# Optimization experiments

Hardware: AMD Instinct MI355X
Metric: run time of the kernel (lower is better)

Reference implementation:

```python
import jax, jax.numpy as jnp
import numpy as np

B, NH, T, H, W = 2, 4, 8, 14, 14
DIM = 384
HD = DIM // NH  # 96 = head_dim = depthwise conv channels
N = T * H * W  # 1568 tokens, no cls
EPS = 1e-6


def _dwconv3d(x, w):
    # x: [BN, C, T, H, W], w: [C, 1, 3, 3, 3]; depthwise conv, stride 1, pad 1
    return jax.lax.conv_general_dilated(
        x, w, window_strides=(1, 1, 1), padding=[(1, 1)] * 3,
        feature_group_count=x.shape[1],
        dimension_numbers=('NCDHW', 'OIDHW', 'NCDHW'))


def _layernorm(x, g, b):
    m = jnp.mean(x, axis=-1, keepdims=True)
    v = jnp.var(x, axis=-1, keepdims=True)
    return (x - m) * jax.lax.rsqrt(v + EPS) * g + b


def _attention_pool(x4, conv_w, ln_g, ln_b, t, h, w):
    # x4: [B, nh, L, c] with L = t*h*w (no cls token)
    Bq, n, L, c = x4.shape
    y = x4.reshape(Bq * n, t, h, w, c).transpose(0, 4, 1, 2, 3)  # [(b nh), c, t, h, w]
    y = _dwconv3d(y, conv_w)
    y = y.transpose(0, 2, 3, 4, 1).reshape(Bq, n, L, c)
    return _layernorm(y, ln_g, ln_b)


def setup_inputs() -> dict:
    key = jax.random.key(0)
    ks = jax.random.split(key, 12)
    inp = {
        'x': jax.random.normal(ks[0], (B, N, DIM), jnp.float32),
        'qkv_w': jax.random.normal(ks[1], (3 * DIM, DIM), jnp.float32) * 0.02,
        'proj_w': jax.random.normal(ks[2], (DIM, DIM), jnp.float32) * 0.02,
        'proj_b': jnp.zeros((DIM,), jnp.float32),
        'pool_q_w': jax.random.normal(ks[3], (HD, 1, 3, 3, 3), jnp.float32) * 0.1,
        'pool_k_w': jax.random.normal(ks[4], (HD, 1, 3, 3, 3), jnp.float32) * 0.1,
        'pool_v_w': jax.random.normal(ks[5], (HD, 1, 3, 3, 3), jnp.float32) * 0.1,
        'norm_q_w': jnp.ones((HD,), jnp.float32), 'norm_q_b': jnp.zeros((HD,), jnp.float32),
        'norm_k_w': jnp.ones((HD,), jnp.float32), 'norm_k_b': jnp.zeros((HD,), jnp.float32),
        'norm_v_w': jnp.ones((HD,), jnp.float32), 'norm_v_b': jnp.zeros((HD,), jnp.float32),
        'rel_pos_h': jax.random.normal(ks[6], (2 * H - 1, HD), jnp.float32) * 0.02,
        'rel_pos_w': jax.random.normal(ks[7], (2 * W - 1, HD), jnp.float32) * 0.02,
        'rel_pos_t': jax.random.normal(ks[8], (2 * T - 1, HD), jnp.float32) * 0.02,
        't': T, 'h': H, 'w': W,
    }
    return inp


def reference(x, qkv_w, proj_w, proj_b, pool_q_w, pool_k_w, pool_v_w,
              norm_q_w, norm_q_b, norm_k_w, norm_k_b, norm_v_w, norm_v_b,
              rel_pos_h, rel_pos_w, rel_pos_t, t, h, w):
    Bq, Nq, _ = x.shape
    # fused QKV projection (qkv_bias=False)
    qkv = (x @ qkv_w.T).reshape(Bq, Nq, 3, NH, HD).transpose(2, 0, 3, 1, 4)
    q, k, v = qkv[0], qkv[1], qkv[2]  # [B, nh, N, hd]
    # pooled Q/K/V: depthwise conv3d + LayerNorm (stride 1 -> shapes preserved)
    q = _attention_pool(q, pool_q_w, norm_q_w, norm_q_b, t, h, w)
    k = _attention_pool(k, pool_k_w, norm_k_w, norm_k_b, t, h, w)
    v = _attention_pool(v, pool_v_w, norm_v_w, norm_v_b, t, h, w)

    scale = HD ** -0.5
    attn = jnp.einsum('bnqc,bnkc->bnqk', q * scale, k)  # [B, nh, N, N]

    # decomposed relative position biases (q_shape == k_shape, ratios == 1)
    dist_h = jnp.arange(h)[:, None] - jnp.arange(h)[None, :] + (h - 1)
    dist_w = jnp.arange(w)[:, None] - jnp.arange(w)[None, :] + (w - 1)
    dist_t = jnp.arange(t)[:, None] - jnp.arange(t)[None, :] + (t - 1)
    Rh = rel_pos_h[dist_h]  # [h, h, c]
    Rw = rel_pos_w[dist_w]  # [w, w, c]
    Rt = rel_pos_t[dist_t]  # [t, t, c]

    r_q = q.reshape(Bq, NH, t, h, w, HD)
    rel_h = jnp.einsum('bnthwc,hkc->bnthwk', r_q, Rh)  # [B,nh,t,h,w,kh]
    rel_w = jnp.einsum('bnthwc,wkc->bnthwk', r_q, Rw)  # [B,nh,t,h,w,kw]
    rel_t = jnp.einsum('bnthwc,tkc->bnthwk', r_q, Rt)  # [B,nh,t,h,w,kt]

    attn8 = attn.reshape(Bq, NH, t, h, w, t, h, w)
    attn8 = (attn8
             + rel_h[:, :, :, :, :, None, :, None]
             + rel_w[:, :, :, :, :, None, None, :]
             + rel_t[:, :, :, :, :, :, None, None])
    attn = jax.nn.softmax(attn8.reshape(Bq, NH, Nq, Nq), axis=-1)

    out = jnp.einsum('bnqk,bnkc->bnqc', attn, v)
    out = out + q  # residual pooling
    out = out.transpose(0, 2, 1, 3).reshape(Bq, Nq, DIM)
    out = out @ proj_w.T + proj_b
    return out
```

## Files before the change

kernel.cpp:

```cpp
#include <hip/hip_runtime.h>

#define B_    2
#define NH_   4
#define T_    8
#define H_    14
#define W_    14
#define HW_   196
#define HD_   96
#define DIM_  384
#define N_    1568
#define BH_   (B_*NH_)
#define BN_   (B_*N_)
#define BHN_  (BH_*N_)
#define CAUG_ 160

typedef unsigned short bf_t;
typedef unsigned int   u32;
typedef __attribute__((ext_vector_type(8))) short bf16x8;
typedef __attribute__((ext_vector_type(4))) float f32x4;

#define LOG2E 1.4426950408889634f
#define QSCALE_LOG2E 0.14724445f

static __device__ __forceinline__ float lo16(u32 v){ union{u32 i; float f;}x; x.i = v<<16;           return x.f; }
static __device__ __forceinline__ float hi16(u32 v){ union{u32 i; float f;}x; x.i = v & 0xffff0000u; return x.f; }
static __device__ __forceinline__ float b2f(bf_t v){ union{u32 i; float f;}x; x.i = ((u32)v)<<16;    return x.f; }
static __device__ __forceinline__ bf_t  f2b(float f){
  union{float f; u32 i;} x; x.f = f;
  return (bf_t)((x.i + 0x7fffu + ((x.i>>16)&1u)) >> 16);
}
static __device__ __forceinline__ u32 pack2(float a, float b){
  return (u32)f2b(a) | ((u32)f2b(b) << 16);
}

#define NA_ (BN_*DIM_)
#define NB_ (3*DIM_*DIM_)
#define NC_ (DIM_*DIM_)
#define CAST_BLOCKS ((NA_+NB_+NC_)/4/256)

__global__ __launch_bounds__(256) void k_cast(
    const float* __restrict__ a, bf_t* __restrict__ ad,
    const float* __restrict__ b, bf_t* __restrict__ bd,
    const float* __restrict__ c, bf_t* __restrict__ cd,
    const float* __restrict__ wq, const float* __restrict__ wk,
    const float* __restrict__ wv, float* __restrict__ tq,
    float* __restrict__ tk, float* __restrict__ tv){
  if (blockIdx.x < CAST_BLOCKS){
    const int i = blockIdx.x*256 + threadIdx.x;
    const int i4 = i*4;
    const float4* src; bf_t* dst; int off;
    if (i4 < NA_)           { src = (const float4*)a; dst = ad; off = i; }
    else if (i4 < NA_+NB_)  { src = (const float4*)b; dst = bd; off = i - NA_/4; }
    else                    { src = (const float4*)c; dst = cd; off = i - (NA_+NB_)/4; }
    const float4 v = src[off];
    ushort4 o; o.x = f2b(v.x); o.y = f2b(v.y); o.z = f2b(v.z); o.w = f2b(v.w);
    ((ushort4*)dst)[off] = o;
  } else {
    const int idx = (blockIdx.x - CAST_BLOCKS)*256 + threadIdx.x;
    if (idx >= 3*HD_*27) return;
    const int t = idx / (HD_*27), rem = idx % (HD_*27);
    const int ch = rem / 27, j = rem % 27;
    const float* s = (t==0)? wq : (t==1)? wk : wv;
    float* d       = (t==0)? tq : (t==1)? tk : tv;
    d[j*HD_ + ch] = s[ch*27 + j];
  }
}

__global__ __launch_bounds__(256) void k_qkv(const bf_t* __restrict__ Xb,
    const bf_t* __restrict__ Wb,
    bf_t* __restrict__ q, bf_t* __restrict__ k, bf_t* __restrict__ v){
  const int wid = threadIdx.x >> 6, lane = threadIdx.x & 63;
  const int wr = wid & 1, wc = wid >> 1;
  const int nl = lane & 15, quad = lane >> 4;
  const int r0 = blockIdx.x*64 + wr*32;
  const int c0 = blockIdx.y*128 + wc*64;
  f32x4 acc[2][4];
  #pragma unroll
  for (int i = 0; i < 2; ++i)
    #pragma unroll
    for (int j = 0; j < 4; ++j) acc[i][j] = (f32x4){0.f,0.f,0.f,0.f};
  const bf_t* A0 = Xb + (size_t)(r0 + nl)*DIM_ + quad*8;
  const bf_t* B0 = Wb + (size_t)(c0 + nl)*DIM_ + quad*8;
  #pragma unroll 2
  for (int k0 = 0; k0 < 12; ++k0){
    const bf16x8 a0 = *(const bf16x8*)(A0 + k0*32);
    const bf16x8 a1 = *(const bf16x8*)(A0 + 16*DIM_ + k0*32);
    bf16x8 bf[4];
    #pragma unroll
    for (int j = 0; j < 4; ++j) bf[j] = *(const bf16x8*)(B0 + (size_t)j*16*DIM_ + k0*32);
    #pragma unroll
    for (int j = 0; j < 4; ++j){
      acc[0][j] = __builtin_amdgcn_mfma_f32_16x16x32_bf16(a0, bf[j], acc[0][j], 0, 0, 0);
      acc[1][j] = __builtin_amdgcn_mfma_f32_16x16x32_bf16(a1, bf[j], acc[1][j], 0, 0, 0);
    }
  }
  #pragma unroll
  for (int i = 0; i < 2; ++i){
    #pragma unroll
    for (int r = 0; r < 4; ++r){
      const int m  = r0 + i*16 + quad*4 + r;
      const int bb = m / N_, nn = m % N_;
      #pragma unroll
      for (int j = 0; j < 4; ++j){
        const int col = c0 + j*16 + nl;
        const int s = col / DIM_, rem = col - s*DIM_;
        const int head = rem / HD_, hc = rem % HD_;
        bf_t* dst = (s==0) ? q : (s==1) ? k : v;
        dst[((size_t)(bb*NH_ + head)*N_ + nn)*HD_ + hc] = f2b(acc[i][j][r]);
      }
    }
  }
}

static __device__ __forceinline__ void ln_butterfly(
    float v0, float v1, float& mean, float& rstd){
  float s  = v0 + v1;
  float s2 = v0*v0 + v1*v1;
  #pragma unroll
  for (int off = 32; off > 0; off >>= 1){
    s  += __shfl_xor(s,  off);
    s2 += __shfl_xor(s2, off);
  }
  mean = s * (1.f/HD_);
  const float var = fmaxf(s2*(1.f/HD_) - mean*mean, 0.f);
  rstd = rsqrtf(var + 1e-6f);
}

__global__ __launch_bounds__(256) void k_pool_slab(
    const bf_t* __restrict__ qr_, const bf_t* __restrict__ kr_, const bf_t* __restrict__ vr_,
    const float* __restrict__ wtq, const float* __restrict__ wtk, const float* __restrict__ wtv,
    const float* __restrict__ gq, const float* __restrict__ bq,
    const float* __restrict__ gk, const float* __restrict__ bk,
    const float* __restrict__ gv, const float* __restrict__ bv,
    const float* __restrict__ rph, const float* __restrict__ rpw,
    const float* __restrict__ rpt,
    bf_t* __restrict__ qp, bf_t* __restrict__ Qaug,
    bf_t* __restrict__ Kt, bf_t* __restrict__ Vtt){
  __shared__ __align__(16) bf_t slab[90][HD_];
  __shared__ float qtmp[4][2][HD_];
  __shared__ u32 vres[8][48];
  const int wid = threadIdx.x >> 6, lane = threadIdx.x & 63;
  const int sec = blockIdx.x / 1568;
  const int rr_ = blockIdx.x % 1568;
  const int bh = rr_ / 196, tok0 = (rr_ % 196)*8;
  const bf_t*  src = (sec==0)? qr_ : (sec==1)? kr_ : vr_;
  const float* wt  = (sec==0)? wtq : (sec==1)? wtk : wtv;
  const float* g   = (sec==0)? gq  : (sec==1)? gk  : gv;
  const float* be  = (sec==0)? bq  : (sec==1)? bk  : bv;
  const bf_t* base = src + (size_t)bh*N_*HD_;

  for (int li = threadIdx.x; li < 90*12; li += 256){
    const int rw = li / 12, ss = li % 12;
    const int dt = rw/30 - 1, dh = (rw%30)/10 - 1, dwp = rw%10 - 1;
    int nn = tok0 + dt*HW_ + dh*W_ + dwp;
    nn = min(max(nn, 0), N_-1);
    *(uint4*)&slab[rw][ss*8] = *(const uint4*)(base + (size_t)nn*HD_ + ss*8);
  }
  __syncthreads();

  const int c0 = (lane < 48) ? 2*lane : 0;
  float2 wgt[27];
  #pragma unroll
  for (int j = 0; j < 27; ++j) wgt[j] = *(const float2*)(wt + j*HD_ + c0);
  const float gg0 = g[c0], gg1 = g[c0+1], be0 = be[c0], be1 = be[c0+1];

  #pragma unroll
  for (int tk = 0; tk < 2; ++tk){
    const int u = wid*2 + tk;
    const int n = tok0 + u;
    const int tt = n / HW_; const int rm = n % HW_;
    const int hh = rm / W_, ww = rm % W_;
    float v0 = 0.f, v1 = 0.f;
    #pragma unroll
    for (int j = 0; j < 27; ++j){
      const int dt = j/9 - 1, dh = (j%9)/3 - 1, dw = j%3 - 1;
      const bool ok = ((unsigned)(tt+dt) < (unsigned)T_)
                   && ((unsigned)(hh+dh) < (unsigned)H_)
                   && ((unsigned)(ww+dw) < (unsigned)W_);
      const int rj = (dt+1)*30 + (dh+1)*10 + (dw + u + 1);
      u32 d = *(const u32*)&slab[rj][c0];
      d = ok ? d : 0u;
      v0 = fmaf(wgt[j].x, lo16(d), v0);
      v1 = fmaf(wgt[j].y, hi16(d), v1);
    }
    if (lane >= 48){ v0 = 0.f; v1 = 0.f; }
    float mean, rstd;
    ln_butterfly(v0, v1, mean, rstd);
    const float y0 = (v0 - mean)*rstd*gg0 + be0;
    const float y1 = (v1 - mean)*rstd*gg1 + be1;

    if (sec == 0){
      const int token = bh*N_ + n;
      if (lane < 48){
        ((u32*)qp)  [(size_t)token*48 + lane] = pack2(y0, y1);
        ((u32*)Qaug)[(size_t)token*80 + lane] = pack2(y0*QSCALE_LOG2E, y1*QSCALE_LOG2E);
        qtmp[wid][tk][c0] = y0; qtmp[wid][tk][c0+1] = y1;
      }
      __syncthreads();
      if (lane < 36){
        const float* tb; int idx;
        if (lane < 14)      { tb = rph; idx = hh - lane      + 13; }
        else if (lane < 28) { tb = rpw; idx = ww - (lane-14) + 13; }
        else                { tb = rpt; idx = tt - (lane-28) +  7; }
        const float4* t4 = (const float4*)(tb + (size_t)idx*HD_);
        float acc = 0.f;
        #pragma unroll
        for (int i = 0; i < 24; ++i){
          const float4 rv = t4[i];
          acc += qtmp[wid][tk][4*i]*rv.x + qtmp[wid][tk][4*i+1]*rv.y
               + qtmp[wid][tk][4*i+2]*rv.z + qtmp[wid][tk][4*i+3]*rv.w;
        }
        Qaug[(size_t)token*CAUG_ + HD_ + lane] = f2b(acc * LOG2E);
      } else if (lane < 64){
        Qaug[(size_t)token*CAUG_ + HD_ + lane] = 0;
      }
    } else if (sec == 1){
      const int tl = n >> 4, nr = n & 15;
      if (lane < 48){
        const size_t idx = ((((size_t)bh*98 + tl)*5 + (lane>>4))*64
                           + ((lane&15)>>2)*16 + nr)*4 + (lane&3);
        ((u32*)Kt)[idx] = pack2(y0, y1);
      } else {
        const int m = lane - 48;
        u32 pr_[2];
        #pragma unroll
        for (int h2 = 0; h2 < 2; ++h2){
          u32 w_ = 0;
          #pragma unroll
          for (int e = 0; e < 2; ++e){
            const int jj = 4*m + 2*h2 + e;
            bool on = (jj < 14) ? (jj == hh) : (jj < 28) ? (jj-14 == ww)
                     : (jj < 36) ? (jj-28 == tt) : false;
            if (on) w_ |= (0x3F80u << (16*e));
          }
          pr_[h2] = w_;
        }
        const size_t bidx = ((((size_t)bh*98 + tl)*5 + (3 + (m>>3)))*64
                            + ((m&7)>>1)*16 + nr)*4 + 2*(m&1);
        *(uint2*)((u32*)Kt + bidx) = make_uint2(pr_[0], pr_[1]);
      }
    } else {
      if (lane < 48) vres[u][lane] = pack2(y0, y1);
    }
  }

  if (sec == 2){
    __syncthreads();
    if (threadIdx.x < HD_){
      const int c = threadIdx.x;
      u32 o[4];
      #pragma unroll
      for (int i = 0; i < 4; ++i){
        const u32 a = vres[2*i][c>>1], b = vres[2*i+1][c>>1];
        const u32 ra = (c&1) ? (a >> 16) : (a & 0xffffu);
        const u32 rb = (c&1) ? (b >> 16) : (b & 0xffffu);
        o[i] = ra | (rb << 16);
      }
      const int pr = tok0 >> 5, qd = (tok0 & 31) >> 3;
      bf_t* dst = Vtt + ((((size_t)bh*49 + pr)*6 + (c>>4))*64 + qd*16 + (c&15))*8;
      *(uint4*)dst = make_uint4(o[0], o[1], o[2], o[3]);
    }
  }
}

__global__ __launch_bounds__(512) void k_attn(
    const bf_t* __restrict__ Qaug, const bf_t* __restrict__ Kt,
    const bf_t* __restrict__ Vtt, const bf_t* __restrict__ qp,
    bf_t* __restrict__ attb){
  __shared__ __align__(16) short Pb[8][16][40];
  __shared__ float Os[8][16][96];
  __shared__ float ms[8][16], ls[8][16];
  const int wid = threadIdx.x >> 6, lane = threadIdx.x & 63;
  const int bh = blockIdx.x / 98, qt = blockIdx.x % 98;
  const int q0 = qt*16;
  const int nl = lane & 15, quad = lane >> 4;

  bf16x8 qa[5];
  {
    const bf_t* Qrow = Qaug + ((size_t)bh*N_ + q0 + nl)*CAUG_ + quad*8;
    #pragma unroll
    for (int i = 0; i < 5; ++i) qa[i] = *(const bf16x8*)(Qrow + i*32);
  }
  short* Pw = &Pb[wid][0][0];

  f32x4 O[6];
  #pragma unroll
  for (int i = 0; i < 6; ++i) O[i] = (f32x4){0.f,0.f,0.f,0.f};
  float mc[4]   = {0.f,0.f,0.f,0.f};
  float rmax[4] = {-3e38f,-3e38f,-3e38f,-3e38f};
  float l[4]    = {0.f,0.f,0.f,0.f};

  auto s_tile = [&](int tl, int half){
    const bf_t* Kp = Kt + (((size_t)bh*98 + tl)*5*64 + lane)*8;
    f32x4 s = (f32x4){0.f,0.f,0.f,0.f};
    #pragma unroll
    for (int i = 0; i < 5; ++i)
      s = __builtin_amdgcn_mfma_f32_16x16x32_bf16(qa[i], *(const bf16x8*)(Kp + i*512), s, 0, 0, 0);
    #pragma unroll
    for (int r = 0; r < 4; ++r){
      rmax[r] = fmaxf(rmax[r], s[r]);
      const float p = exp2f(s[r] - mc[r]);
      l[r] += p;
      Pw[(quad*4 + r)*40 + half*16 + nl] = (short)f2b(p);
    }
  };
  auto rescale = [&](){
    #pragma unroll
    for (int r = 0; r < 4; ++r){
      float tm = rmax[r];
      tm = fmaxf(tm, __shfl_xor(tm, 1));
      tm = fmaxf(tm, __shfl_xor(tm, 2));
      tm = fmaxf(tm, __shfl_xor(tm, 4));
      tm = fmaxf(tm, __shfl_xor(tm, 8));
      const float mn = fmaxf(mc[r], tm);
      const float al = exp2f(mc[r] - mn);
      mc[r] = mn; l[r] *= al;
      #pragma unroll
      for (int ct = 0; ct < 6; ++ct) O[ct][r] *= al;
    }
  };

  const int p0 = (wid == 0) ? 0 : (7 + 6*(wid-1));
  const int npairs = (wid == 0) ? 7 : 6;
  #pragma unroll 1
  for (int pi = 0; pi < npairs; ++pi){
    const int kp = p0 + pi;
    s_tile(2*kp,     0);
    s_tile(2*kp + 1, 1);
    const bf16x8 pa = *(const bf16x8*)(Pw + nl*40 + quad*8);
    const bf_t* Vp = Vtt + (((size_t)bh*49 + kp)*6*64 + lane)*8;
    #pragma unroll
    for (int ct = 0; ct < 6; ++ct)
      O[ct] = __builtin_amdgcn_mfma_f32_16x16x32_bf16(pa, *(const bf16x8*)(Vp + ct*512), O[ct], 0, 0, 0);
    if (pi == npairs-1) rescale();
  }

  #pragma unroll
  for (int r = 0; r < 4; ++r){
    float ls_ = l[r];
    ls_ += __shfl_xor(ls_, 1); ls_ += __shfl_xor(ls_, 2);
    ls_ += __shfl_xor(ls_, 4); ls_ += __shfl_xor(ls_, 8);
    if (nl == 0){ ms[wid][quad*4 + r] = mc[r]; ls[wid][quad*4 + r] = ls_; }
    #pragma unroll
    for (int ct = 0; ct < 6; ++ct) Os[wid][quad*4 + r][ct*16 + nl] = O[ct][r];
  }
  __syncthreads();

  const int bb = bh >> 2, head = bh & 3;
  for (int e = threadIdx.x; e < 16*96; e += 512){
    const int row = e / 96, col = e % 96;
    float mx = -3e38f;
    #pragma unroll
    for (int w = 0; w < 8; ++w) mx = fmaxf(mx, ms[w][row]);
    float L = 0.f, A = 0.f;
    #pragma unroll
    for (int w = 0; w < 8; ++w){
      const float wt = exp2f(ms[w][row] - mx);
      L += wt*ls[w][row];
      A += wt*Os[w][row][col];
    }
    const int qg = q0 + row;
    const float val = A/L + b2f(qp[((size_t)bh*N_ + qg)*HD_ + col]);
    attb[((size_t)(bb*N_ + qg))*DIM_ + head*HD_ + col] = f2b(val);
  }
}

__global__ __launch_bounds__(256) void k_proj(const bf_t* __restrict__ Ab,
    const bf_t* __restrict__ Wpb, const float* __restrict__ pb,
    float* __restrict__ out){
  const int wid = threadIdx.x >> 6, lane = threadIdx.x & 63;
  const int wr = wid & 1, wc = wid >> 1;
  const int nl = lane & 15, quad = lane >> 4;
  const int r0 = blockIdx.x*64 + wr*32;
  const int c0 = blockIdx.y*128 + wc*64;
  f32x4 acc[2][4];
  #pragma unroll
  for (int i = 0; i < 2; ++i)
    #pragma unroll
    for (int j = 0; j < 4; ++j) acc[i][j] = (f32x4){0.f,0.f,0.f,0.f};
  const bf_t* A0 = Ab  + (size_t)(r0 + nl)*DIM_ + quad*8;
  const bf_t* B0 = Wpb + (size_t)(c0 + nl)*DIM_ + quad*8;
  #pragma unroll 2
  for (int k0 = 0; k0 < 12; ++k0){
    const bf16x8 a0 = *(const bf16x8*)(A0 + k0*32);
    const bf16x8 a1 = *(const bf16x8*)(A0 + 16*DIM_ + k0*32);
    bf16x8 bf[4];
    #pragma unroll
    for (int j = 0; j < 4; ++j) bf[j] = *(const bf16x8*)(B0 + (size_t)j*16*DIM_ + k0*32);
    #pragma unroll
    for (int j = 0; j < 4; ++j){
      acc[0][j] = __builtin_amdgcn_mfma_f32_16x16x32_bf16(a0, bf[j], acc[0][j], 0, 0, 0);
      acc[1][j] = __builtin_amdgcn_mfma_f32_16x16x32_bf16(a1, bf[j], acc[1][j], 0, 0, 0);
    }
  }
  #pragma unroll
  for (int i = 0; i < 2; ++i){
    #pragma unroll
    for (int r = 0; r < 4; ++r){
      const int m = r0 + i*16 + quad*4 + r;
      #pragma unroll
      for (int j = 0; j < 4; ++j){
        const int col = c0 + j*16 + nl;
        out[(size_t)m*DIM_ + col] = acc[i][j][r] + pb[col];
      }
    }
  }
}

extern "C" void kernel_launch(void* const* d_in, const int* in_sizes, int n_in,
                              void* d_out, int out_size, void* d_ws, size_t ws_size,
                              hipStream_t stream){
  const float* x      = (const float*)d_in[0];
  const float* qkv_w  = (const float*)d_in[1];
  const float* proj_w = (const float*)d_in[2];
  const float* proj_b = (const float*)d_in[3];
  const float* pqw    = (const float*)d_in[4];
  const float* pkw    = (const float*)d_in[5];
  const float* pvw    = (const float*)d_in[6];
  const float* nqw    = (const float*)d_in[7];
  const float* nqb    = (const float*)d_in[8];
  const float* nkw    = (const float*)d_in[9];
  const float* nkb    = (const float*)d_in[10];
  const float* nvw    = (const float*)d_in[11];
  const float* nvb    = (const float*)d_in[12];
  const float* rph    = (const float*)d_in[13];
  const float* rpw    = (const float*)d_in[14];
  const float* rpt    = (const float*)d_in[15];

  char* p = (char*)d_ws;
  const size_t RAW = (size_t)BH_*N_*HD_*2;
  const size_t AUG = (size_t)BH_*N_*CAUG_*2;
  bf_t* xb     = (bf_t*)(p);
  bf_t* wqkvb  = (bf_t*)(p + RAW);
  bf_t* wprojb = (bf_t*)(p + RAW + 884736);
  char* p2 = p + RAW + 884736 + 294912;
  bf_t* raw_q  = (bf_t*)(p2);
  bf_t* raw_k  = (bf_t*)(p2 + RAW);
  bf_t* raw_v  = (bf_t*)(p2 + 2*RAW);
  bf_t* attb   = raw_q;
  bf_t* qp     = (bf_t*)(p2 + 3*RAW);
  bf_t* Qaug   = (bf_t*)(p2 + 4*RAW);
  bf_t* Kt     = (bf_t*)(p2 + 4*RAW + AUG);
  bf_t* Vtt    = (bf_t*)(p2 + 4*RAW + 2*AUG);
  float* wtq   = (float*)(p2 + 4*RAW + 2*AUG + RAW);
  float* wtk   = wtq + 27*HD_;
  float* wtv   = wtk + 27*HD_;

  k_cast     <<<CAST_BLOCKS + 31, 256, 0, stream>>>(x, xb, qkv_w, wqkvb, proj_w, wprojb,
                                                    pqw, pkw, pvw, wtq, wtk, wtv);
  k_qkv      <<<dim3(BN_/64, 9),  256, 0, stream>>>(xb, wqkvb, raw_q, raw_k, raw_v);
  k_pool_slab<<<3*1568,           256, 0, stream>>>(raw_q, raw_k, raw_v,
                                                    wtq, wtk, wtv,
                                                    nqw, nqb, nkw, nkb, nvw, nvb,
                                                    rph, rpw, rpt,
                                                    qp, Qaug, Kt, Vtt);
  k_attn     <<<BH_*98,           512, 0, stream>>>(Qaug, Kt, Vtt, qp, attb);
  k_proj     <<<dim3(BN_/64, 3),  256, 0, stream>>>(attb, wprojb, proj_b, (float*)d_out);
}
```

Before: 221.1 us.

## Store GEMM operands in MFMA fragment-tiled layout and pool 16 tokens per block

```diff
diff --git a/kernel.cpp b/kernel.cpp
--- a/kernel.cpp
+++ b/kernel.cpp
@@ -32,6 +32,9 @@
 static __device__ __forceinline__ u32 pack2(float a, float b){
   return (u32)f2b(a) | ((u32)f2b(b) << 16);
 }
+static __device__ __forceinline__ size_t ftidx(int row, int k){
+  return ((((size_t)(row>>4))*12 + (k>>5))*64 + ((k>>3)&3)*16 + (row&15))*8 + (k&7);
+}
 
 #define NA_ (BN_*DIM_)
 #define NB_ (3*DIM_*DIM_)
@@ -48,13 +51,21 @@
   if (blockIdx.x < CAST_BLOCKS){
     const int i = blockIdx.x*256 + threadIdx.x;
     const int i4 = i*4;
-    const float4* src; bf_t* dst; int off;
-    if (i4 < NA_)           { src = (const float4*)a; dst = ad; off = i; }
-    else if (i4 < NA_+NB_)  { src = (const float4*)b; dst = bd; off = i - NA_/4; }
-    else                    { src = (const float4*)c; dst = cd; off = i - (NA_+NB_)/4; }
-    const float4 v = src[off];
+    float4 v; bf_t* dst; int row, k;
+    if (i4 < NA_){
+      v = ((const float4*)a)[i];
+      dst = ad; row = i4/DIM_; k = i4%DIM_;
+    } else if (i4 < NA_+NB_){
+      const int f = i4 - NA_;
+      v = ((const float4*)b)[i - NA_/4];
+      dst = bd; row = f/DIM_; k = f%DIM_;
+    } else {
+      const int f = i4 - NA_ - NB_;
+      v = ((const float4*)c)[i - (NA_+NB_)/4];
+      dst = cd; row = f/DIM_; k = f%DIM_;
+    }
     ushort4 o; o.x = f2b(v.x); o.y = f2b(v.y); o.z = f2b(v.z); o.w = f2b(v.w);
-    ((ushort4*)dst)[off] = o;
+    *(ushort4*)(dst + ftidx(row, k)) = o;
   } else {
     const int idx = (blockIdx.x - CAST_BLOCKS)*256 + threadIdx.x;
     if (idx >= 3*HD_*27) return;
@@ -66,28 +77,29 @@
   }
 }
 
-__global__ __launch_bounds__(256) void k_qkv(const bf_t* __restrict__ Xb,
-    const bf_t* __restrict__ Wb,
+__global__ __launch_bounds__(256) void k_qkv(const bf_t* __restrict__ Xt,
+    const bf_t* __restrict__ Wt,
     bf_t* __restrict__ q, bf_t* __restrict__ k, bf_t* __restrict__ v){
   const int wid = threadIdx.x >> 6, lane = threadIdx.x & 63;
   const int wr = wid & 1, wc = wid >> 1;
   const int nl = lane & 15, quad = lane >> 4;
   const int r0 = blockIdx.x*64 + wr*32;
-  const int c0 = blockIdx.y*128 + wc*64;
+  const int mt0 = r0 >> 4;
+  const int nt0 = blockIdx.y*8 + wc*4;
   f32x4 acc[2][4];
   #pragma unroll
   for (int i = 0; i < 2; ++i)
     #pragma unroll
     for (int j = 0; j < 4; ++j) acc[i][j] = (f32x4){0.f,0.f,0.f,0.f};
-  const bf_t* A0 = Xb + (size_t)(r0 + nl)*DIM_ + quad*8;
-  const bf_t* B0 = Wb + (size_t)(c0 + nl)*DIM_ + quad*8;
+  const bf_t* A0 = Xt + ((size_t)mt0*12*64 + lane)*8;
+  const bf_t* B0 = Wt + ((size_t)nt0*12*64 + lane)*8;
   #pragma unroll 2
   for (int k0 = 0; k0 < 12; ++k0){
-    const bf16x8 a0 = *(const bf16x8*)(A0 + k0*32);
-    const bf16x8 a1 = *(const bf16x8*)(A0 + 16*DIM_ + k0*32);
+    const bf16x8 a0 = *(const bf16x8*)(A0 + k0*512);
+    const bf16x8 a1 = *(const bf16x8*)(A0 + 12*512 + k0*512);
     bf16x8 bf[4];
     #pragma unroll
-    for (int j = 0; j < 4; ++j) bf[j] = *(const bf16x8*)(B0 + (size_t)j*16*DIM_ + k0*32);
+    for (int j = 0; j < 4; ++j) bf[j] = *(const bf16x8*)(B0 + (size_t)(j*12 + k0)*512);
     #pragma unroll
     for (int j = 0; j < 4; ++j){
       acc[0][j] = __builtin_amdgcn_mfma_f32_16x16x32_bf16(a0, bf[j], acc[0][j], 0, 0, 0);
@@ -102,7 +114,7 @@
       const int bb = m / N_, nn = m % N_;
       #pragma unroll
       for (int j = 0; j < 4; ++j){
-        const int col = c0 + j*16 + nl;
+        const int col = (nt0 + j)*16 + nl;
         const int s = col / DIM_, rem = col - s*DIM_;
         const int head = rem / HD_, hc = rem % HD_;
         bf_t* dst = (s==0) ? q : (s==1) ? k : v;
@@ -136,23 +148,23 @@
     const float* __restrict__ rpt,
     bf_t* __restrict__ qp, bf_t* __restrict__ Qaug,
     bf_t* __restrict__ Kt, bf_t* __restrict__ Vtt){
-  __shared__ __align__(16) bf_t slab[90][HD_];
-  __shared__ float qtmp[4][2][HD_];
-  __shared__ u32 vres[8][48];
+  __shared__ __align__(16) bf_t slab[162][HD_];
+  __shared__ float qtmp[4][4][HD_];
+  __shared__ u32 vres[16][48];
   const int wid = threadIdx.x >> 6, lane = threadIdx.x & 63;
-  const int sec = blockIdx.x / 1568;
-  const int rr_ = blockIdx.x % 1568;
-  const int bh = rr_ / 196, tok0 = (rr_ % 196)*8;
+  const int sec = blockIdx.x / 784;
+  const int rr_ = blockIdx.x % 784;
+  const int bh = rr_ / 98, tok0 = (rr_ % 98)*16;
   const bf_t*  src = (sec==0)? qr_ : (sec==1)? kr_ : vr_;
   const float* wt  = (sec==0)? wtq : (sec==1)? wtk : wtv;
   const float* g   = (sec==0)? gq  : (sec==1)? gk  : gv;
   const float* be  = (sec==0)? bq  : (sec==1)? bk  : bv;
   const bf_t* base = src + (size_t)bh*N_*HD_;
 
-  for (int li = threadIdx.x; li < 90*12; li += 256){
+  for (int li = threadIdx.x; li < 162*12; li += 256){
     const int rw = li / 12, ss = li % 12;
-    const int dt = rw/30 - 1, dh = (rw%30)/10 - 1, dwp = rw%10 - 1;
-    int nn = tok0 + dt*HW_ + dh*W_ + dwp;
+    const int aa = rw/54, bb2 = (rw%54)/18, cc = rw%18;
+    int nn = tok0 + (aa-1)*HW_ + (bb2-1)*W_ + (cc-1);
     nn = min(max(nn, 0), N_-1);
     *(uint4*)&slab[rw][ss*8] = *(const uint4*)(base + (size_t)nn*HD_ + ss*8);
   }
@@ -164,9 +176,9 @@
   for (int j = 0; j < 27; ++j) wgt[j] = *(const float2*)(wt + j*HD_ + c0);
   const float gg0 = g[c0], gg1 = g[c0+1], be0 = be[c0], be1 = be[c0+1];
 
-  #pragma unroll
-  for (int tk = 0; tk < 2; ++tk){
-    const int u = wid*2 + tk;
+  #pragma unroll 1
+  for (int tk = 0; tk < 4; ++tk){
+    const int u = wid*4 + tk;
     const int n = tok0 + u;
     const int tt = n / HW_; const int rm = n % HW_;
     const int hh = rm / W_, ww = rm % W_;
@@ -177,7 +189,7 @@
       const bool ok = ((unsigned)(tt+dt) < (unsigned)T_)
                    && ((unsigned)(hh+dh) < (unsigned)H_)
                    && ((unsigned)(ww+dw) < (unsigned)W_);
-      const int rj = (dt+1)*30 + (dh+1)*10 + (dw + u + 1);
+      const int rj = (dt+1)*54 + (dh+1)*18 + (dw + u + 1);
       u32 d = *(const u32*)&slab[rj][c0];
       d = ok ? d : 0u;
       v0 = fmaf(wgt[j].x, lo16(d), v0);
@@ -246,17 +258,19 @@
 
   if (sec == 2){
     __syncthreads();
-    if (threadIdx.x < HD_){
-      const int c = threadIdx.x;
+    if (threadIdx.x < 2*HD_){
+      const int grp = threadIdx.x / HD_, c = threadIdx.x % HD_;
+      const int t0g = grp*8;
       u32 o[4];
       #pragma unroll
       for (int i = 0; i < 4; ++i){
-        const u32 a = vres[2*i][c>>1], b = vres[2*i+1][c>>1];
+        const u32 a = vres[t0g + 2*i][c>>1], b = vres[t0g + 2*i+1][c>>1];
         const u32 ra = (c&1) ? (a >> 16) : (a & 0xffffu);
         const u32 rb = (c&1) ? (b >> 16) : (b & 0xffffu);
         o[i] = ra | (rb << 16);
       }
-      const int pr = tok0 >> 5, qd = (tok0 & 31) >> 3;
+      const int n0g = tok0 + t0g;
+      const int pr = n0g >> 5, qd = (n0g & 31) >> 3;
       bf_t* dst = Vtt + ((((size_t)bh*49 + pr)*6 + (c>>4))*64 + qd*16 + (c&15))*8;
       *(uint4*)dst = make_uint4(o[0], o[1], o[2], o[3]);
     }
@@ -347,6 +361,7 @@
   __syncthreads();
 
   const int bb = bh >> 2, head = bh & 3;
+  const int grow0 = bb*N_ + q0;
   for (int e = threadIdx.x; e < 16*96; e += 512){
     const int row = e / 96, col = e % 96;
     float mx = -3e38f;
@@ -359,34 +374,34 @@
       L += wt*ls[w][row];
       A += wt*Os[w][row][col];
     }
-    const int qg = q0 + row;
-    const float val = A/L + b2f(qp[((size_t)bh*N_ + qg)*HD_ + col]);
-    attb[((size_t)(bb*N_ + qg))*DIM_ + head*HD_ + col] = f2b(val);
-  }
-}
-
-__global__ __launch_bounds__(256) void k_proj(const bf_t* __restrict__ Ab,
-    const bf_t* __restrict__ Wpb, const float* __restrict__ pb,
+    const float val = A/L + b2f(qp[((size_t)bh*N_ + q0 + row)*HD_ + col]);
+    attb[ftidx(grow0 + row, head*HD_ + col)] = f2b(val);
+  }
+}
+
+__global__ __launch_bounds__(256) void k_proj(const bf_t* __restrict__ At,
+    const bf_t* __restrict__ Wpt, const float* __restrict__ pb,
     float* __restrict__ out){
   const int wid = threadIdx.x >> 6, lane = threadIdx.x & 63;
   const int wr = wid & 1, wc = wid >> 1;
   const int nl = lane & 15, quad = lane >> 4;
   const int r0 = blockIdx.x*64 + wr*32;
-  const int c0 = blockIdx.y*128 + wc*64;
+  const int mt0 = r0 >> 4;
+  const int nt0 = blockIdx.y*8 + wc*4;
   f32x4 acc[2][4];
   #pragma unroll
   for (int i = 0; i < 2; ++i)
     #pragma unroll
     for (int j = 0; j < 4; ++j) acc[i][j] = (f32x4){0.f,0.f,0.f,0.f};
-  const bf_t* A0 = Ab  + (size_t)(r0 + nl)*DIM_ + quad*8;
-  const bf_t* B0 = Wpb + (size_t)(c0 + nl)*DIM_ + quad*8;
+  const bf_t* A0 = At  + ((size_t)mt0*12*64 + lane)*8;
+  const bf_t* B0 = Wpt + ((size_t)nt0*12*64 + lane)*8;
   #pragma unroll 2
   for (int k0 = 0; k0 < 12; ++k0){
-    const bf16x8 a0 = *(const bf16x8*)(A0 + k0*32);
-    const bf16x8 a1 = *(const bf16x8*)(A0 + 16*DIM_ + k0*32);
+    const bf16x8 a0 = *(const bf16x8*)(A0 + k0*512);
+    const bf16x8 a1 = *(const bf16x8*)(A0 + 12*512 + k0*512);
     bf16x8 bf[4];
     #pragma unroll
-    for (int j = 0; j < 4; ++j) bf[j] = *(const bf16x8*)(B0 + (size_t)j*16*DIM_ + k0*32);
+    for (int j = 0; j < 4; ++j) bf[j] = *(const bf16x8*)(B0 + (size_t)(j*12 + k0)*512);
     #pragma unroll
     for (int j = 0; j < 4; ++j){
       acc[0][j] = __builtin_amdgcn_mfma_f32_16x16x32_bf16(a0, bf[j], acc[0][j], 0, 0, 0);
@@ -400,7 +415,7 @@
       const int m = r0 + i*16 + quad*4 + r;
       #pragma unroll
       for (int j = 0; j < 4; ++j){
-        const int col = c0 + j*16 + nl;
+        const int col = (nt0 + j)*16 + nl;
         out[(size_t)m*DIM_ + col] = acc[i][j][r] + pb[col];
       }
     }
@@ -449,7 +464,7 @@
   k_cast     <<<CAST_BLOCKS + 31, 256, 0, stream>>>(x, xb, qkv_w, wqkvb, proj_w, wprojb,
                                                     pqw, pkw, pvw, wtq, wtk, wtv);
   k_qkv      <<<dim3(BN_/64, 9),  256, 0, stream>>>(xb, wqkvb, raw_q, raw_k, raw_v);
-  k_pool_slab<<<3*1568,           256, 0, stream>>>(raw_q, raw_k, raw_v,
+  k_pool_slab<<<3*784,            256, 0, stream>>>(raw_q, raw_k, raw_v,
                                                     wtq, wtk, wtv,
                                                     nqw, nqb, nkw, nkb, nvw, nvb,
                                                     rph, rpw, rpt,
```

Result: faster. 205.6 us (-7.0%).
